# Kernel optimization log

Measured on AMD Instinct MI355X. Metric: run time of the kernel, lower is better.

The kernel has to match this reference:

```python
import jax, jax.numpy as jnp
import numpy as np

DIM = 1024
N_HEADS = 16
HEAD_DIM = DIM // N_HEADS


def setup_inputs() -> dict:
    key = jax.random.key(0)
    k_x, k_qkv, k_out = jax.random.split(key, 3)
    B, T = 4, 2048
    x = jax.random.normal(k_x, (B, T, DIM), dtype=jnp.float32)
    W_qkv = jax.random.normal(k_qkv, (DIM, 3 * DIM), dtype=jnp.float32) * 0.02
    b_qkv = jnp.zeros((3 * DIM,), dtype=jnp.float32)
    W_out = jax.random.normal(k_out, (DIM, DIM), dtype=jnp.float32) * 0.02
    b_out = jnp.zeros((DIM,), dtype=jnp.float32)
    return {"x": x, "W_qkv": W_qkv, "b_qkv": b_qkv, "W_out": W_out, "b_out": b_out}


def reference(x, W_qkv, b_qkv, W_out, b_out):
    B, T, C = x.shape
    qkv = x @ W_qkv + b_qkv  # (B, T, 3C)
    q, k, v = jnp.split(qkv, 3, axis=-1)
    # (B, H, T, D)
    q = q.reshape(B, T, N_HEADS, HEAD_DIM).transpose(0, 2, 1, 3)
    k = k.reshape(B, T, N_HEADS, HEAD_DIM).transpose(0, 2, 1, 3)
    v = v.reshape(B, T, N_HEADS, HEAD_DIM).transpose(0, 2, 1, 3)
    scale = 1.0 / jnp.sqrt(jnp.asarray(HEAD_DIM, dtype=x.dtype))
    scores = jnp.einsum('bhqd,bhkd->bhqk', q, k) * scale  # (B, H, T, T)
    causal = jnp.tril(jnp.ones((T, T), dtype=bool))  # True = allowed
    scores = jnp.where(causal, scores, jnp.asarray(-jnp.inf, dtype=scores.dtype))
    attn = jax.nn.softmax(scores, axis=-1)
    out = jnp.einsum('bhqk,bhkd->bhqd', attn, v)  # (B, H, T, D)
    out = out.transpose(0, 2, 1, 3).reshape(B, T, C)
    return out @ W_out + b_out
```

## Files before the change

### kernel.cpp

```cpp
#include <hip/hip_runtime.h>
#include <hip/hip_bf16.h>
#include <cstdint>
#include <cstddef>

#define DIM   1024
#define NH    16
#define HD    64
#define BB    4
#define TT    2048

typedef __attribute__((ext_vector_type(8))) short bf16x8;
typedef __attribute__((ext_vector_type(4))) short bf16x4;
typedef __attribute__((ext_vector_type(4))) float f32x4;
typedef __attribute__((ext_vector_type(4))) unsigned short u16x4;
typedef unsigned short u16;
typedef unsigned int u32;

#define NEG_INF (-__builtin_inff())
#define QSCALE 0.18033688011110543f
#define AS1 __attribute__((address_space(1)))
#define AS3 __attribute__((address_space(3)))

static __device__ __forceinline__ u16 f2bf(float f) {
  union { float f; unsigned u; } v; v.f = f;
  return (u16)((v.u + 0x7FFFu + ((v.u >> 16) & 1u)) >> 16);
}

static __device__ __forceinline__ u16 bfbits(float a) {
  union { __hip_bfloat16 h; u16 u; } c; c.h = __float2bfloat16(a); return c.u;
}
static __device__ __forceinline__ u32 pk_bf16(float a, float b) {
  return (u32)bfbits(a) | ((u32)bfbits(b) << 16);
}

static __device__ __forceinline__ float exp2_fast(float x) {
  float r;
  asm("v_exp_f32 %0, %1" : "=v"(r) : "v"(x));
  return r;
}

static __device__ __forceinline__ bf16x4 tr16(u32 byte_addr) {
  bf16x4 d;
  asm volatile("ds_read_b64_tr_b16 %0, %1" : "=v"(d) : "v"(byte_addr));
  return d;
}

__global__ __launch_bounds__(256) void k_cvt(const float* __restrict__ in,
                                             u16* __restrict__ out, int n4) {
  int i = blockIdx.x * 256 + threadIdx.x;
  if (i >= n4) return;
  float4 v = reinterpret_cast<const float4*>(in)[i];
  u16x4 o = { f2bf(v.x), f2bf(v.y), f2bf(v.z), f2bf(v.w) };
  *reinterpret_cast<u16x4*>(out + (size_t)i * 4) = o;
}

__global__ __launch_bounds__(256) void k_transpose(const float* __restrict__ in,
                                                   u16* __restrict__ out,
                                                   int R, int C) {
  __shared__ float tile[32][33];
  int bx = blockIdx.x * 32;
  int by = blockIdx.y * 32;
  int tx = threadIdx.x & 31, ty = threadIdx.x >> 5;
  #pragma unroll
  for (int i = 0; i < 32; i += 8)
    tile[ty + i][tx] = in[(size_t)(by + ty + i) * C + bx + tx];
  __syncthreads();
  #pragma unroll
  for (int i = 0; i < 32; i += 8)
    out[(size_t)(bx + ty + i) * R + by + tx] = f2bf(tile[tx][ty + i]);
}

template <int OUT_BF16>
__global__ __launch_bounds__(256, 2) void k_gemm(const u16* __restrict__ A,
                                                 const u16* __restrict__ Bt,
                                                 const float* __restrict__ bias,
                                                 u16* __restrict__ Cb,
                                                 float* __restrict__ Cf,
                                                 int M, int N, int K,
                                                 int scale_cols, float scale) {
  __shared__ __align__(16) u16 lA[2][128 * 32];
  __shared__ __align__(16) u16 lB[2][128 * 32];
  const int tid = threadIdx.x;
  const int m0 = blockIdx.y * 128, n0 = blockIdx.x * 128;
  const int lane = tid & 63;
  const int w = tid >> 6;
  const int g = lane >> 4, r = lane & 15;
  const int wm = w >> 1, wn = w & 1;

  f32x4 acc[4][4] = {};

  const int KT = K >> 5;

  auto stage = [&](int buf, int kt) {
    const int k0 = kt << 5;
    #pragma unroll
    for (int i = 0; i < 2; ++i) {
      int c = tid + 256 * i;
      int row = c >> 2, col = (c & 3) << 3;
      const u16* gp = A + (size_t)(m0 + row) * K + k0 + col;
      u16* lp = &lA[buf][c << 3];
      __builtin_amdgcn_global_load_lds((const AS1 void*)gp, (AS3 void*)lp, 16, 0, 0);
    }
    #pragma unroll
    for (int i = 0; i < 2; ++i) {
      int c = tid + 256 * i;
      int row = c >> 2, col = (c & 3) << 3;
      const u16* gp = Bt + (size_t)(n0 + row) * K + k0 + col;
      u16* lp = &lB[buf][c << 3];
      __builtin_amdgcn_global_load_lds((const AS1 void*)gp, (AS3 void*)lp, 16, 0, 0);
    }
  };

  stage(0, 0);
  asm volatile("s_waitcnt vmcnt(0)" ::: "memory");
  __syncthreads();

  int cur = 0;
  for (int kt = 0; kt < KT; ++kt) {
    if (kt + 1 < KT) stage(cur ^ 1, kt + 1);
    bf16x8 af[4], bfr[4];
    #pragma unroll
    for (int m = 0; m < 4; ++m)
      af[m] = *(const bf16x8*)&lA[cur][(wm * 64 + m * 16 + r) * 32 + g * 8];
    #pragma unroll
    for (int n = 0; n < 4; ++n)
      bfr[n] = *(const bf16x8*)&lB[cur][(wn * 64 + n * 16 + r) * 32 + g * 8];
    #pragma unroll
    for (int m = 0; m < 4; ++m)
      #pragma unroll
      for (int n = 0; n < 4; ++n)
        acc[m][n] = __builtin_amdgcn_mfma_f32_16x16x32_bf16(af[m], bfr[n], acc[m][n], 0, 0, 0);
    asm volatile("s_waitcnt vmcnt(0)" ::: "memory");
    __syncthreads();
    cur ^= 1;
  }

  #pragma unroll
  for (int n = 0; n < 4; ++n) {
    int col = n0 + wn * 64 + n * 16 + r;
    float bv = bias[col];
    float sc = (col < scale_cols) ? scale : 1.0f;
    #pragma unroll
    for (int m = 0; m < 4; ++m) {
      #pragma unroll
      for (int reg = 0; reg < 4; ++reg) {
        int row = m0 + wm * 64 + m * 16 + g * 4 + reg;
        float val = (acc[m][n][reg] + bv) * sc;
        if (OUT_BF16) Cb[(size_t)row * N + col] = f2bf(val);
        else          Cf[(size_t)row * N + col] = val;
      }
    }
  }
}

#define KVB 64
#define LBUF16 8192

__global__ __launch_bounds__(256, 2) void k_attn(const u16* __restrict__ qkv,
                                                 u16* __restrict__ aout) {
  __shared__ __align__(16) u16 smem[2 * LBUF16];

  const int bid = blockIdx.x;
  const int swz = (bid & 7) * 64 + (bid >> 3);
  const int bh = swz >> 3;
  const int p = swz & 7;
  const int b = bh >> 4, h = bh & 15;
  const int tid = threadIdx.x, w = tid >> 6, lane = tid & 63;
  const int g = lane >> 4, r = lane & 15;

  const u32 vls0 = (u32)(uintptr_t)(AS3 u16*)(smem + 4096);
  const u32 vls1 = (u32)(uintptr_t)(AS3 u16*)(smem + LBUF16 + 4096);

  auto issueKV = [&](int buf, int t) {
    const int kv0 = t * KVB;
    u16* kb = &smem[buf * LBUF16];
    u16* vb = &smem[buf * LBUF16 + 4096];
    #pragma unroll
    for (int i = 0; i < 2; ++i) {
      int s = tid + 256 * i;
      int row = s >> 3, c8 = s & 7;
      int colg = c8 ^ (row & 7);
      const u16* gp = qkv + ((size_t)(b * TT) + kv0 + row) * (3 * DIM) + DIM + h * HD + colg * 8;
      __builtin_amdgcn_global_load_lds((const AS1 void*)gp,
                                       (AS3 void*)(kb + (size_t)s * 8), 16, 0, 0);
    }
    #pragma unroll
    for (int i = 0; i < 2; ++i) {
      int s = tid + 256 * i;
      int key = (s >> 1) & 63;
      int c = ((s >> 7) << 1) | (s & 1);
      const u16* gp = qkv + ((size_t)(b * TT) + kv0 + key) * (3 * DIM) + 2 * DIM + h * HD + c * 8;
      __builtin_amdgcn_global_load_lds((const AS1 void*)gp,
                                       (AS3 void*)(vb + (size_t)s * 8), 16, 0, 0);
    }
  };

  for (int half = 0; half < 2; ++half) {
    const int qt = half ? p : (15 - p);
    const int qbase = qt * 128;
    const int nt = 2 * qt + 2;
    const int qg0 = qbase + w * 16 + r;

    bf16x8 qf[2][2];
    #pragma unroll
    for (int qb = 0; qb < 2; ++qb) {
      const u16* qp = qkv + ((size_t)(b * TT) + qg0 + qb * 64) * (3 * DIM) + h * HD;
      #pragma unroll
      for (int kk = 0; kk < 2; ++kk)
        qf[qb][kk] = *(const bf16x8*)&qp[kk * 32 + g * 8];
    }

    f32x4 o[2][4] = {};
    float mrow[2] = { NEG_INF, NEG_INF };
    float lrow[2] = { 0.f, 0.f };

    issueKV(0, 0);
    issueKV(1, 1);
    __syncthreads();

    int cur = 0;
    for (int t = 0; t < nt; ++t) {
      const bool last = (t == nt - 1);
      const bool pen  = (t == nt - 2);
      const bool do0  = !last;
      const int kv0 = t * KVB;
      const u16* lk = &smem[cur * LBUF16];

      f32x4 s0[4] = {}, s1[4] = {};
      __builtin_amdgcn_s_setprio(1);
      #pragma unroll
      for (int c = 0; c < 4; ++c) {
        const int row = c * 16 + r;
        const int sw = (r & 7) << 3;
        bf16x8 kf0 = *(const bf16x8*)&lk[(row * 64 + g * 8) ^ sw];
        bf16x8 kf1 = *(const bf16x8*)&lk[(row * 64 + 32 + g * 8) ^ sw];
        if (do0) {
          s0[c] = __builtin_amdgcn_mfma_f32_16x16x32_bf16(kf0, qf[0][0], s0[c], 0, 0, 0);
          s0[c] = __builtin_amdgcn_mfma_f32_16x16x32_bf16(kf1, qf[0][1], s0[c], 0, 0, 0);
        }
        s1[c] = __builtin_amdgcn_mfma_f32_16x16x32_bf16(kf0, qf[1][0], s1[c], 0, 0, 0);
        s1[c] = __builtin_amdgcn_mfma_f32_16x16x32_bf16(kf1, qf[1][1], s1[c], 0, 0, 0);
      }
      __builtin_amdgcn_s_setprio(0);

      bf16x8 pf0[2], pf1[2];
      auto softmax = [&](f32x4* s, float& mref, float& lref, f32x4* ov,
                         bf16x8* pf, bool msk, int qg) {
        float pv[16];
        #pragma unroll
        for (int c = 0; c < 4; ++c)
          #pragma unroll
          for (int e = 0; e < 4; ++e) {
            float sv = s[c][e];
            if (msk) {
              int key = kv0 + c * 16 + g * 4 + e;
              if (key > qg) sv = NEG_INF;
            }
            pv[c * 4 + e] = sv;
          }
        float t8[8];
        #pragma unroll
        for (int i = 0; i < 8; ++i) t8[i] = fmaxf(pv[i], pv[i + 8]);
        #pragma unroll
        for (int i = 0; i < 4; ++i) t8[i] = fmaxf(t8[i], t8[i + 4]);
        float tm = fmaxf(fmaxf(t8[0], t8[1]), fmaxf(t8[2], t8[3]));
        tm = fmaxf(tm, __shfl_xor(tm, 16));
        tm = fmaxf(tm, __shfl_xor(tm, 32));
        if (__any(tm > mref + 8.0f)) {
          float mn = fmaxf(mref, tm);
          float corr = exp2_fast(mref - mn);
          lref *= corr;
          #pragma unroll
          for (int cd = 0; cd < 4; ++cd) ov[cd] *= corr;
          mref = mn;
        }
        #pragma unroll
        for (int i = 0; i < 16; ++i) pv[i] = exp2_fast(pv[i] - mref);
        float a8[8];
        #pragma unroll
        for (int i = 0; i < 8; ++i) a8[i] = pv[i] + pv[i + 8];
        #pragma unroll
        for (int i = 0; i < 4; ++i) a8[i] = a8[i] + a8[i + 4];
        float ps = (a8[0] + a8[1]) + (a8[2] + a8[3]);
        ps += __shfl_xor(ps, 16);
        ps += __shfl_xor(ps, 32);
        lref += ps;
        union { bf16x8 v; u32 w[4]; } u0, u1;
        #pragma unroll
        for (int k = 0; k < 4; ++k) {
          u0.w[k] = pk_bf16(pv[2 * k], pv[2 * k + 1]);
          u1.w[k] = pk_bf16(pv[8 + 2 * k], pv[9 + 2 * k]);
        }
        pf[0] = u0.v; pf[1] = u1.v;
      };
      if (do0) softmax(s0, mrow[0], lrow[0], o[0], pf0, pen, qg0);
      softmax(s1, mrow[1], lrow[1], o[1], pf1, last, qg0 + 64);

      bf16x4 tr[4][4];
      const u32 vb = (cur ? vls1 : vls0) + (u32)lane * 8;
      #pragma unroll
      for (int cd = 0; cd < 4; ++cd)
        #pragma unroll
        for (int kh = 0; kh < 4; ++kh)
          tr[cd][kh] = tr16(vb + cd * 2048 + kh * 512);
      asm volatile("s_waitcnt lgkmcnt(0)" ::: "memory");
      __builtin_amdgcn_sched_barrier(0);
      __builtin_amdgcn_s_setprio(1);
      #pragma unroll
      for (int cd = 0; cd < 4; ++cd) {
        #pragma unroll
        for (int ks = 0; ks < 2; ++ks) {
          bf16x4 lo = tr[cd][ks * 2], hi = tr[cd][ks * 2 + 1];
          bf16x8 av = { lo[0], lo[1], lo[2], lo[3], hi[0], hi[1], hi[2], hi[3] };
          if (do0) o[0][cd] = __builtin_amdgcn_mfma_f32_16x16x32_bf16(av, pf0[ks], o[0][cd], 0, 0, 0);
          o[1][cd] = __builtin_amdgcn_mfma_f32_16x16x32_bf16(av, pf1[ks], o[1][cd], 0, 0, 0);
        }
      }
      __builtin_amdgcn_s_setprio(0);

      __syncthreads();
      if (t + 2 < nt) issueKV(cur, t + 2);
      cur ^= 1;
    }

    #pragma unroll
    for (int qb = 0; qb < 2; ++qb) {
      const float inv = 1.0f / lrow[qb];
      u16* op = aout + ((size_t)(b * TT) + qg0 + qb * 64) * DIM + h * HD;
      #pragma unroll
      for (int cd = 0; cd < 4; ++cd) {
        union { u16x4 v; u32 w[2]; } pk;
        pk.w[0] = pk_bf16(o[qb][cd][0] * inv, o[qb][cd][1] * inv);
        pk.w[1] = pk_bf16(o[qb][cd][2] * inv, o[qb][cd][3] * inv);
        *(u16x4*)&op[cd * 16 + g * 4] = pk.v;
      }
    }
  }
}

extern "C" void kernel_launch(void* const* d_in, const int* in_sizes, int n_in,
                              void* d_out, int out_size, void* d_ws, size_t ws_size,
                              hipStream_t stream) {
  const float* x    = (const float*)d_in[0];
  const float* Wqkv = (const float*)d_in[1];
  const float* bqkv = (const float*)d_in[2];
  const float* Wout = (const float*)d_in[3];
  const float* bout = (const float*)d_in[4];
  float* out = (float*)d_out;

  const int M = BB * TT;
  u16* xb   = (u16*)d_ws;
  u16* wqt  = xb + (size_t)M * DIM;
  u16* wot  = wqt + (size_t)3 * DIM * DIM;
  u16* qkvb = wot + (size_t)DIM * DIM;
  u16* aob  = qkvb + (size_t)M * 3 * DIM;

  k_cvt<<<(M * DIM / 4 + 255) / 256, 256, 0, stream>>>(x, xb, M * DIM / 4);
  k_transpose<<<dim3(3 * DIM / 32, DIM / 32), 256, 0, stream>>>(Wqkv, wqt, DIM, 3 * DIM);
  k_transpose<<<dim3(DIM / 32, DIM / 32), 256, 0, stream>>>(Wout, wot, DIM, DIM);

  k_gemm<1><<<dim3(3 * DIM / 128, M / 128), 256, 0, stream>>>(
      xb, wqt, bqkv, qkvb, nullptr, M, 3 * DIM, DIM, DIM, QSCALE);

  k_attn<<<BB * NH * 8, 256, 0, stream>>>(qkvb, aob);

  k_gemm<0><<<dim3(DIM / 128, M / 128), 256, 0, stream>>>(
      aob, wot, bout, nullptr, out, M, DIM, DIM, 0, 1.0f);
}
```

Before: 178.9 us.

## Replace QKV GEMM with 256x256-tile 8-wave kernel using direct-to-LDS loads

Adds a new GEMM kernel for the QKV projection that uses 256x256 output tiles with 512 threads and a 64-wide K step. It loads tiles straight from global memory into LDS with an XOR swizzle and double buffering, and interleaves LDS reads, MFMAs and prefetches under barriers. Workgroup indices are remapped so tiles are grouped per XCD for L2 reuse. The larger tile raises arithmetic intensity, but it leaves only 384 workgroups and increases register pressure.

```diff
diff --git a/kernel.cpp b/kernel.cpp
--- a/kernel.cpp
+++ b/kernel.cpp
@@ -68,6 +68,137 @@
   #pragma unroll
   for (int i = 0; i < 32; i += 8)
     out[(size_t)(bx + ty + i) * R + by + tx] = f2bf(tile[tx][ty + i]);
+}
+
+template <int OUT_BF16>
+__global__ __launch_bounds__(512, 2) void k_gemm256(const u16* __restrict__ A,
+                                                    const u16* __restrict__ Bt,
+                                                    const float* __restrict__ bias,
+                                                    u16* __restrict__ Cb,
+                                                    float* __restrict__ Cf,
+                                                    int M, int N, int K,
+                                                    int scale_cols, float scale,
+                                                    int nbx) {
+  __shared__ __align__(16) u16 lds[2][2][2][8192];
+
+  const int tid = threadIdx.x;
+  const int nwg = gridDim.x;
+  const int q = nwg >> 3, rm = nwg & 7;
+  const int xcd = blockIdx.x & 7, lidx = blockIdx.x >> 3;
+  const int swz = (xcd < rm ? xcd * (q + 1) : rm * (q + 1) + (xcd - rm) * q) + lidx;
+  const int m0 = (swz / nbx) * 256, n0 = (swz % nbx) * 256;
+
+  const int w = tid >> 6, lane = tid & 63;
+  const int g = lane >> 4, r = lane & 15;
+  const int wm = w >> 2, wn = w & 3;
+
+  f32x4 acc[8][4] = {};
+  const int KT = K >> 6;
+
+  auto stageA = [&](int buf, int h, int kt) {
+    char* base = (char*)&lds[buf][0][h][0];
+    #pragma unroll
+    for (int i = 0; i < 2; ++i) {
+      int o = (tid + i * 512) * 16;
+      int l = o ^ (((o >> 9) & 1) << 5);
+      int row = (l >> 6) & 127, ks = l >> 13, kb = l & 63;
+      const u16* gp = A + (size_t)(m0 + h * 128 + row) * K + kt * 64 + ks * 32 + (kb >> 1);
+      __builtin_amdgcn_global_load_lds((const AS1 void*)gp, (AS3 void*)(base + o), 16, 0, 0);
+    }
+  };
+  auto stageB = [&](int buf, int h, int kt) {
+    char* base = (char*)&lds[buf][1][h][0];
+    #pragma unroll
+    for (int i = 0; i < 2; ++i) {
+      int o = (tid + i * 512) * 16;
+      int l = o ^ (((o >> 9) & 1) << 5);
+      int row = (l >> 6) & 127, ks = l >> 13, kb = l & 63;
+      const u16* gp = Bt + (size_t)(n0 + h * 128 + row) * K + kt * 64 + ks * 32 + (kb >> 1);
+      __builtin_amdgcn_global_load_lds((const AS1 void*)gp, (AS3 void*)(base + o), 16, 0, 0);
+    }
+  };
+
+  auto ldA = [&](int buf, int qm, bf16x8 (&a)[4][2]) {
+    const char* base = (const char*)&lds[buf][0][wm][0];
+    #pragma unroll
+    for (int f = 0; f < 4; ++f)
+      #pragma unroll
+      for (int ks = 0; ks < 2; ++ks) {
+        int l = ks * 8192 + (qm * 64 + f * 16 + r) * 64 + g * 16;
+        int ph = l ^ (((l >> 9) & 1) << 5);
+        a[f][ks] = *(const bf16x8*)(base + ph);
+      }
+  };
+  auto ldB = [&](int buf, int qn, bf16x8 (&bb)[2][2]) {
+    const char* base = (const char*)&lds[buf][1][wn >> 1][0];
+    #pragma unroll
+    for (int c = 0; c < 2; ++c)
+      #pragma unroll
+      for (int ks = 0; ks < 2; ++ks) {
+        int l = ks * 8192 + ((wn & 1) * 64 + qn * 32 + c * 16 + r) * 64 + g * 16;
+        int ph = l ^ (((l >> 9) & 1) << 5);
+        bb[c][ks] = *(const bf16x8*)(base + ph);
+      }
+  };
+  auto mfma16 = [&](bf16x8 (&a)[4][2], bf16x8 (&bb)[2][2], int rf0, int cf0) {
+    __builtin_amdgcn_s_setprio(1);
+    #pragma unroll
+    for (int f = 0; f < 4; ++f)
+      #pragma unroll
+      for (int c = 0; c < 2; ++c)
+        #pragma unroll
+        for (int ks = 0; ks < 2; ++ks)
+          acc[rf0 + f][cf0 + c] = __builtin_amdgcn_mfma_f32_16x16x32_bf16(
+              a[f][ks], bb[c][ks], acc[rf0 + f][cf0 + c], 0, 0, 0);
+    __builtin_amdgcn_s_setprio(0);
+  };
+
+  stageA(0, 0, 0); stageA(0, 1, 0); stageB(0, 0, 0); stageB(0, 1, 0);
+  stageA(1, 0, 1); stageA(1, 1, 1); stageB(1, 0, 1); stageB(1, 1, 1);
+  asm volatile("s_waitcnt vmcnt(8)" ::: "memory");
+  __builtin_amdgcn_s_barrier();
+
+  bf16x8 af[4][2], b0[2][2], b1[2][2];
+  for (int kt = 0; kt < KT; ++kt) {
+    const int buf = kt & 1;
+    const bool st = (kt + 2 < KT);
+    ldA(buf, 0, af);
+    ldB(buf, 0, b0);
+    __builtin_amdgcn_s_barrier();
+    mfma16(af, b0, 0, 0);
+    __builtin_amdgcn_s_barrier();
+    ldB(buf, 1, b1);
+    __builtin_amdgcn_s_barrier();
+    mfma16(af, b1, 0, 2);
+    __builtin_amdgcn_s_barrier();
+    ldA(buf, 1, af);
+    if (st) { stageB(buf, 0, kt + 2); stageB(buf, 1, kt + 2); }
+    __builtin_amdgcn_s_barrier();
+    mfma16(af, b1, 4, 2);
+    __builtin_amdgcn_s_barrier();
+    if (st) { stageA(buf, 0, kt + 2); stageA(buf, 1, kt + 2); }
+    mfma16(af, b0, 4, 0);
+    if (st) asm volatile("s_waitcnt vmcnt(8)" ::: "memory");
+    else    asm volatile("s_waitcnt vmcnt(0)" ::: "memory");
+    __builtin_amdgcn_s_barrier();
+  }
+
+  #pragma unroll
+  for (int cf = 0; cf < 4; ++cf) {
+    int col = n0 + wn * 64 + cf * 16 + r;
+    float bv = bias[col];
+    float sc = (col < scale_cols) ? scale : 1.0f;
+    #pragma unroll
+    for (int rf = 0; rf < 8; ++rf) {
+      #pragma unroll
+      for (int e = 0; e < 4; ++e) {
+        int row = m0 + wm * 128 + rf * 16 + g * 4 + e;
+        float val = (acc[rf][cf][e] + bv) * sc;
+        if (OUT_BF16) Cb[(size_t)row * N + col] = f2bf(val);
+        else          Cf[(size_t)row * N + col] = val;
+      }
+    }
+  }
 }
 
 template <int OUT_BF16>
@@ -359,8 +490,8 @@
   k_transpose<<<dim3(3 * DIM / 32, DIM / 32), 256, 0, stream>>>(Wqkv, wqt, DIM, 3 * DIM);
   k_transpose<<<dim3(DIM / 32, DIM / 32), 256, 0, stream>>>(Wout, wot, DIM, DIM);
 
-  k_gemm<1><<<dim3(3 * DIM / 128, M / 128), 256, 0, stream>>>(
-      xb, wqt, bqkv, qkvb, nullptr, M, 3 * DIM, DIM, DIM, QSCALE);
+  k_gemm256<1><<<(M / 256) * (3 * DIM / 256), 512, 0, stream>>>(
+      xb, wqt, bqkv, qkvb, nullptr, M, 3 * DIM, DIM, DIM, QSCALE, 3 * DIM / 256);
 
   k_attn<<<BB * NH * 8, 256, 0, stream>>>(qkvb, aob);
 
```

Measured after the change: 184.3 us. +3.0%, slower.

## Rewrite GEMM as 256x128-tile 8-wave kernel with triple-buffered A and XCD swizzle

Applied to the files above, without the earlier changes.

Replaces the 128x128, 4-wave, double-buffered GEMM with a 512-thread kernel computing 256x128 tiles. The K step is 64 and A is triple-buffered, B double-buffered, with an XOR-swizzled LDS layout. Loads are split into two phases interleaved with MFMA bursts under s_setprio, and blocks are remapped so neighbouring tiles land on the same XCD. The aim is better latency hiding and operand reuse in both projection GEMMs, at the cost of 128KB of LDS per block and more barriers.

```diff
diff --git a/kernel.cpp b/kernel.cpp
--- a/kernel.cpp
+++ b/kernel.cpp
@@ -44,6 +44,8 @@
   asm volatile("ds_read_b64_tr_b16 %0, %1" : "=v"(d) : "v"(byte_addr));
   return d;
 }
+
+#define MFMA16(A, B, C) __builtin_amdgcn_mfma_f32_16x16x32_bf16(A, B, C, 0, 0, 0)
 
 __global__ __launch_bounds__(256) void k_cvt(const float* __restrict__ in,
                                              u16* __restrict__ out, int n4) {
@@ -71,81 +73,125 @@
 }
 
 template <int OUT_BF16>
-__global__ __launch_bounds__(256, 2) void k_gemm(const u16* __restrict__ A,
-                                                 const u16* __restrict__ Bt,
-                                                 const float* __restrict__ bias,
-                                                 u16* __restrict__ Cb,
-                                                 float* __restrict__ Cf,
-                                                 int M, int N, int K,
-                                                 int scale_cols, float scale) {
-  __shared__ __align__(16) u16 lA[2][128 * 32];
-  __shared__ __align__(16) u16 lB[2][128 * 32];
+__global__ __launch_bounds__(512, 2) void k_gemm8p(const u16* __restrict__ A,
+                                                   const u16* __restrict__ Bt,
+                                                   const float* __restrict__ bias,
+                                                   u16* __restrict__ Cb,
+                                                   float* __restrict__ Cf,
+                                                   int M, int N, int K,
+                                                   int scale_cols, float scale,
+                                                   int nbx) {
+  __shared__ __align__(16) char lds[131072];
+
   const int tid = threadIdx.x;
-  const int m0 = blockIdx.y * 128, n0 = blockIdx.x * 128;
-  const int lane = tid & 63;
-  const int w = tid >> 6;
+  const int nwg = gridDim.x;
+  const int qq = nwg >> 3, rm = nwg & 7;
+  const int xcd = blockIdx.x & 7, lidx = blockIdx.x >> 3;
+  const int swz = (xcd < rm ? xcd * (qq + 1) : rm * (qq + 1) + (xcd - rm) * qq) + lidx;
+  const int m0 = (swz / nbx) * 256, n0 = (swz % nbx) * 128;
+
+  const int w = tid >> 6, lane = tid & 63;
   const int g = lane >> 4, r = lane & 15;
   const int wm = w >> 1, wn = w & 1;
 
   f32x4 acc[4][4] = {};
-
-  const int KT = K >> 5;
-
-  auto stage = [&](int buf, int kt) {
-    const int k0 = kt << 5;
+  const int KT = K >> 6;
+
+  auto stageH = [&](char* base, const u16* src, int grow0, int kt) {
     #pragma unroll
     for (int i = 0; i < 2; ++i) {
-      int c = tid + 256 * i;
-      int row = c >> 2, col = (c & 3) << 3;
-      const u16* gp = A + (size_t)(m0 + row) * K + k0 + col;
-      u16* lp = &lA[buf][c << 3];
-      __builtin_amdgcn_global_load_lds((const AS1 void*)gp, (AS3 void*)lp, 16, 0, 0);
-    }
-    #pragma unroll
-    for (int i = 0; i < 2; ++i) {
-      int c = tid + 256 * i;
-      int row = c >> 2, col = (c & 3) << 3;
-      const u16* gp = Bt + (size_t)(n0 + row) * K + k0 + col;
-      u16* lp = &lB[buf][c << 3];
-      __builtin_amdgcn_global_load_lds((const AS1 void*)gp, (AS3 void*)lp, 16, 0, 0);
-    }
-  };
-
-  stage(0, 0);
-  asm volatile("s_waitcnt vmcnt(0)" ::: "memory");
-  __syncthreads();
-
-  int cur = 0;
-  for (int kt = 0; kt < KT; ++kt) {
-    if (kt + 1 < KT) stage(cur ^ 1, kt + 1);
-    bf16x8 af[4], bfr[4];
-    #pragma unroll
-    for (int m = 0; m < 4; ++m)
-      af[m] = *(const bf16x8*)&lA[cur][(wm * 64 + m * 16 + r) * 32 + g * 8];
-    #pragma unroll
-    for (int n = 0; n < 4; ++n)
-      bfr[n] = *(const bf16x8*)&lB[cur][(wn * 64 + n * 16 + r) * 32 + g * 8];
-    #pragma unroll
-    for (int m = 0; m < 4; ++m)
-      #pragma unroll
-      for (int n = 0; n < 4; ++n)
-        acc[m][n] = __builtin_amdgcn_mfma_f32_16x16x32_bf16(af[m], bfr[n], acc[m][n], 0, 0, 0);
-    asm volatile("s_waitcnt vmcnt(0)" ::: "memory");
-    __syncthreads();
-    cur ^= 1;
+      int o = (tid + i * 512) * 16;
+      int l = o ^ (((o >> 9) & 1) << 5);
+      int row = (l >> 6) & 127, ks = l >> 13, kb = l & 63;
+      const u16* gp = src + (size_t)(grow0 + row) * K + kt * 64 + ks * 32 + (kb >> 1);
+      __builtin_amdgcn_global_load_lds((const AS1 void*)gp, (AS3 void*)(base + o), 16, 0, 0);
+    }
+  };
+  auto stageA = [&](int t) {
+    char* ab = lds + (t % 3) * 32768;
+    stageH(ab, A, m0, t);
+    stageH(ab + 16384, A, m0 + 128, t);
+  };
+  auto stageB = [&](int t) {
+    stageH(lds + 98304 + (t & 1) * 16384, Bt, n0, t);
+  };
+
+  auto ldAf = [&](int t, int f, bf16x8 (&dst)[2]) {
+    const char* base = lds + (t % 3) * 32768 + (wm >> 1) * 16384;
+    int rowb = ((wm & 1) * 64 + f * 16 + r) * 64 + g * 16;
+    #pragma unroll
+    for (int ks = 0; ks < 2; ++ks) {
+      int l = ks * 8192 + rowb;
+      dst[ks] = *(const bf16x8*)(base + (l ^ (((l >> 9) & 1) << 5)));
+    }
+  };
+  auto ldBf = [&](int t, int c, bf16x8 (&dst)[2]) {
+    const char* base = lds + 98304 + (t & 1) * 16384;
+    int rowb = (wn * 64 + c * 16 + r) * 64 + g * 16;
+    #pragma unroll
+    for (int ks = 0; ks < 2; ++ks) {
+      int l = ks * 8192 + rowb;
+      dst[ks] = *(const bf16x8*)(base + (l ^ (((l >> 9) & 1) << 5)));
+    }
+  };
+
+  stageA(0); stageB(0); stageA(1); stageB(1);
+  asm volatile("s_waitcnt vmcnt(6)" ::: "memory");
+  __builtin_amdgcn_s_barrier();
+
+  for (int t = 0; t < KT; ++t) {
+    const bool st = (t + 2 < KT);
+    bf16x8 a0[2], a1[2], a2[2], a3[2], b0[2], b1[2], b2[2], b3[2];
+    ldAf(t, 0, a0); ldAf(t, 1, a1);
+    ldBf(t, 0, b0); ldBf(t, 1, b1); ldBf(t, 2, b2); ldBf(t, 3, b3);
+    if (st) stageA(t + 2);
+    __builtin_amdgcn_s_barrier();
+    __builtin_amdgcn_s_setprio(1);
+    #pragma unroll
+    for (int ks = 0; ks < 2; ++ks) {
+      acc[0][0] = MFMA16(a0[ks], b0[ks], acc[0][0]);
+      acc[0][1] = MFMA16(a0[ks], b1[ks], acc[0][1]);
+      acc[0][2] = MFMA16(a0[ks], b2[ks], acc[0][2]);
+      acc[0][3] = MFMA16(a0[ks], b3[ks], acc[0][3]);
+      acc[1][0] = MFMA16(a1[ks], b0[ks], acc[1][0]);
+      acc[1][1] = MFMA16(a1[ks], b1[ks], acc[1][1]);
+      acc[1][2] = MFMA16(a1[ks], b2[ks], acc[1][2]);
+      acc[1][3] = MFMA16(a1[ks], b3[ks], acc[1][3]);
+    }
+    __builtin_amdgcn_s_setprio(0);
+    __builtin_amdgcn_s_barrier();
+    ldAf(t, 2, a2); ldAf(t, 3, a3);
+    if (st) stageB(t + 2);
+    __builtin_amdgcn_s_barrier();
+    __builtin_amdgcn_s_setprio(1);
+    #pragma unroll
+    for (int ks = 0; ks < 2; ++ks) {
+      acc[2][0] = MFMA16(a2[ks], b0[ks], acc[2][0]);
+      acc[2][1] = MFMA16(a2[ks], b1[ks], acc[2][1]);
+      acc[2][2] = MFMA16(a2[ks], b2[ks], acc[2][2]);
+      acc[2][3] = MFMA16(a2[ks], b3[ks], acc[2][3]);
+      acc[3][0] = MFMA16(a3[ks], b0[ks], acc[3][0]);
+      acc[3][1] = MFMA16(a3[ks], b1[ks], acc[3][1]);
+      acc[3][2] = MFMA16(a3[ks], b2[ks], acc[3][2]);
+      acc[3][3] = MFMA16(a3[ks], b3[ks], acc[3][3]);
+    }
+    __builtin_amdgcn_s_setprio(0);
+    if (st) asm volatile("s_waitcnt vmcnt(6)" ::: "memory");
+    else    asm volatile("s_waitcnt vmcnt(0)" ::: "memory");
+    __builtin_amdgcn_s_barrier();
   }
 
   #pragma unroll
-  for (int n = 0; n < 4; ++n) {
-    int col = n0 + wn * 64 + n * 16 + r;
+  for (int c = 0; c < 4; ++c) {
+    int col = n0 + wn * 64 + c * 16 + r;
     float bv = bias[col];
     float sc = (col < scale_cols) ? scale : 1.0f;
     #pragma unroll
-    for (int m = 0; m < 4; ++m) {
-      #pragma unroll
-      for (int reg = 0; reg < 4; ++reg) {
-        int row = m0 + wm * 64 + m * 16 + g * 4 + reg;
-        float val = (acc[m][n][reg] + bv) * sc;
+    for (int f = 0; f < 4; ++f) {
+      #pragma unroll
+      for (int e = 0; e < 4; ++e) {
+        int row = m0 + wm * 64 + f * 16 + g * 4 + e;
+        float val = (acc[f][c][e] + bv) * sc;
         if (OUT_BF16) Cb[(size_t)row * N + col] = f2bf(val);
         else          Cf[(size_t)row * N + col] = val;
       }
@@ -235,11 +281,11 @@
         bf16x8 kf0 = *(const bf16x8*)&lk[(row * 64 + g * 8) ^ sw];
         bf16x8 kf1 = *(const bf16x8*)&lk[(row * 64 + 32 + g * 8) ^ sw];
         if (do0) {
-          s0[c] = __builtin_amdgcn_mfma_f32_16x16x32_bf16(kf0, qf[0][0], s0[c], 0, 0, 0);
-          s0[c] = __builtin_amdgcn_mfma_f32_16x16x32_bf16(kf1, qf[0][1], s0[c], 0, 0, 0);
+          s0[c] = MFMA16(kf0, qf[0][0], s0[c]);
+          s0[c] = MFMA16(kf1, qf[0][1], s0[c]);
         }
-        s1[c] = __builtin_amdgcn_mfma_f32_16x16x32_bf16(kf0, qf[1][0], s1[c], 0, 0, 0);
-        s1[c] = __builtin_amdgcn_mfma_f32_16x16x32_bf16(kf1, qf[1][1], s1[c], 0, 0, 0);
+        s1[c] = MFMA16(kf0, qf[1][0], s1[c]);
+        s1[c] = MFMA16(kf1, qf[1][1], s1[c]);
       }
       __builtin_amdgcn_s_setprio(0);
 
@@ -312,8 +358,8 @@
         for (int ks = 0; ks < 2; ++ks) {
           bf16x4 lo = tr[cd][ks * 2], hi = tr[cd][ks * 2 + 1];
           bf16x8 av = { lo[0], lo[1], lo[2], lo[3], hi[0], hi[1], hi[2], hi[3] };
-          if (do0) o[0][cd] = __builtin_amdgcn_mfma_f32_16x16x32_bf16(av, pf0[ks], o[0][cd], 0, 0, 0);
-          o[1][cd] = __builtin_amdgcn_mfma_f32_16x16x32_bf16(av, pf1[ks], o[1][cd], 0, 0, 0);
+          if (do0) o[0][cd] = MFMA16(av, pf0[ks], o[0][cd]);
+          o[1][cd] = MFMA16(av, pf1[ks], o[1][cd]);
         }
       }
       __builtin_amdgcn_s_setprio(0);
@@ -359,11 +405,11 @@
   k_transpose<<<dim3(3 * DIM / 32, DIM / 32), 256, 0, stream>>>(Wqkv, wqt, DIM, 3 * DIM);
   k_transpose<<<dim3(DIM / 32, DIM / 32), 256, 0, stream>>>(Wout, wot, DIM, DIM);
 
-  k_gemm<1><<<dim3(3 * DIM / 128, M / 128), 256, 0, stream>>>(
-      xb, wqt, bqkv, qkvb, nullptr, M, 3 * DIM, DIM, DIM, QSCALE);
+  k_gemm8p<1><<<(M / 256) * (3 * DIM / 128), 512, 0, stream>>>(
+      xb, wqt, bqkv, qkvb, nullptr, M, 3 * DIM, DIM, DIM, QSCALE, 3 * DIM / 128);
 
   k_attn<<<BB * NH * 8, 256, 0, stream>>>(qkvb, aob);
 
-  k_gemm<0><<<dim3(DIM / 128, M / 128), 256, 0, stream>>>(
-      aob, wot, bout, nullptr, out, M, DIM, DIM, 0, 1.0f);
-}
+  k_gemm8p<0><<<(M / 256) * (DIM / 128), 512, 0, stream>>>(
+      aob, wot, bout, nullptr, out, M, DIM, DIM, 0, 1.0f, DIM / 128);
+}
```

After: 169.5 us. -5.3%, faster.
